# Performance work log

Hardware: AMD Instinct MI355X
Metric: run time of the kernel (lower is better)

## Reference

```python
import jax, jax.numpy as jnp
import numpy as np

N, E, D, H = 50000, 400000, 128, 256


def setup_inputs() -> dict:
    key = jax.random.key(0)
    ks = jax.random.split(key, 16)
    s = 0.02
    inp = {
        "x": jax.random.normal(ks[0], (N, D), dtype=jnp.float32),
        "edge_index": jax.random.randint(ks[1], (2, E), 0, N, dtype=jnp.int64),
        "steps": 1,
        # encoder MLP: Linear(D->H), Linear(H->H), relu after each
        "enc_w1": jax.random.normal(ks[2], (H, D), dtype=jnp.float32) * s,
        "enc_b1": jnp.zeros((H,), dtype=jnp.float32),
        "enc_w2": jax.random.normal(ks[3], (H, H), dtype=jnp.float32) * s,
        "enc_b2": jnp.zeros((H,), dtype=jnp.float32),
        # GeneralConv lin_msg (root_weight=False, bias=True)
        "msg_w": jax.random.normal(ks[4], (H, H), dtype=jnp.float32) * s,
        "msg_b": jnp.zeros((H,), dtype=jnp.float32),
        # decoder MLP: Linear(2H->H) relu, Linear(H->D) tanh
        "dec_w1": jax.random.normal(ks[5], (H, 2 * H), dtype=jnp.float32) * s,
        "dec_b1": jnp.zeros((H,), dtype=jnp.float32),
        "dec_w2": jax.random.normal(ks[6], (D, H), dtype=jnp.float32) * s,
        "dec_b2": jnp.zeros((D,), dtype=jnp.float32),
    }
    return inp


def reference(x, edge_index, steps, enc_w1, enc_b1, enc_w2, enc_b2,
              msg_w, msg_b, dec_w1, dec_b1, dec_w2, dec_b2):
    src = edge_index[0]
    dst = edge_index[1]
    n = x.shape[0]
    for _ in range(steps):  # steps is a small static python int
        # encoder MLP (batch_norm=False, dropout=0, relu + relu)
        h = jax.nn.relu(x @ enc_w1.T + enc_b1)
        h = jax.nn.relu(h @ enc_w2.T + enc_b2)
        # GeneralConv: message = lin_msg(x_j); aggr='add'; no root weight
        # lin_msg is edge-independent -> transform on nodes, then gather/scatter
        m = h @ msg_w.T + msg_b                      # [N, H]
        out = jax.ops.segment_sum(m[src], dst, num_segments=n)  # [N, H]
        # decoder on cat(out, h): relu then tanh
        d = jax.nn.relu(jnp.concatenate([out, h], axis=-1) @ dec_w1.T + dec_b1)
        x = jnp.tanh(d @ dec_w2.T + dec_b2)
    return x
```

## Files before the change

kernel.cpp:

```cpp
#include <hip/hip_runtime.h>
#include <cmath>


typedef __attribute__((ext_vector_type(8))) short  short8;
typedef __attribute__((ext_vector_type(4))) float  f32x4;
typedef __attribute__((ext_vector_type(4))) unsigned short us4;

typedef unsigned short u16;
typedef unsigned int   u32;

static __device__ __forceinline__ u16 f2bf(float f) {
    u32 u = __float_as_uint(f);
    u = (u + 0x7FFFu + ((u >> 16) & 1u)) >> 16;
    return (u16)u;
}
static __device__ __forceinline__ float bf2f(u16 h) {
    return __uint_as_float(((u32)h) << 16);
}

static __device__ __forceinline__ void g2l16(const void* g, void* l) {
    __builtin_amdgcn_global_load_lds(
        (const __attribute__((address_space(1))) u32*)g,
        (__attribute__((address_space(3))) u32*)l, 16, 0, 0);
}

__global__ __launch_bounds__(512, 2) void enc_fused(
    const u16* __restrict__ xb, const u16* __restrict__ w1,
    const float* __restrict__ b1, const u16* __restrict__ w2,
    const float* __restrict__ b2, const u16* __restrict__ wm,
    const float* __restrict__ bm, u16* __restrict__ hout,
    u16* __restrict__ mout, const int N)
{
    __shared__ u16 As[64 * 32];
    __shared__ u16 Ws[256 * 32];
    __shared__ u16 hL[8][64 * 32];

    const int t    = threadIdx.x;
    const int r0   = blockIdx.x * 64;
    const int wave = t >> 6;
    const int lane = t & 63;
    const int n    = lane & 15;
    const int q    = lane >> 4;
    const int wc   = wave * 32;
    const int lrow = lane >> 2;
    const int qofs = (lane & 3) * 8;

    const int arow = min(r0 + wave * 16 + lrow, N - 1);
    const u16* aptr = xb + (size_t)arow * 128 + qofs;
    const int wrA = wave * 16 + lrow;
    const int wrB = (wave + 8) * 16 + lrow;

    f32x4 acc[4][2];
#pragma unroll
    for (int i = 0; i < 4; i++)
#pragma unroll
        for (int j = 0; j < 2; j++) acc[i][j] = (f32x4)0.0f;

    for (int kc = 0; kc < 128; kc += 32) {
        __syncthreads();
        if (wave < 4) g2l16(aptr + kc, &As[wave * 512]);
        g2l16(w1 + (size_t)wrA * 128 + kc + qofs, &Ws[wave * 512]);
        g2l16(w1 + (size_t)wrB * 128 + kc + qofs, &Ws[(wave + 8) * 512]);
        __syncthreads();
        short8 af[4], bf[2];
#pragma unroll
        for (int i = 0; i < 4; i++)
            af[i] = *reinterpret_cast<const short8*>(&As[(i * 16 + n) * 32 + q * 8]);
#pragma unroll
        for (int j = 0; j < 2; j++)
            bf[j] = *reinterpret_cast<const short8*>(&Ws[(wc + j * 16 + n) * 32 + q * 8]);
#pragma unroll
        for (int i = 0; i < 4; i++)
#pragma unroll
            for (int j = 0; j < 2; j++)
                acc[i][j] = __builtin_amdgcn_mfma_f32_16x16x32_bf16(
                    af[i], bf[j], acc[i][j], 0, 0, 0);
    }
    {
        float bv[2];
#pragma unroll
        for (int j = 0; j < 2; j++) bv[j] = b1[wc + j * 16 + n];
#pragma unroll
        for (int i = 0; i < 4; i++)
#pragma unroll
            for (int reg = 0; reg < 4; reg++) {
                const int row = i * 16 + q * 4 + reg;
#pragma unroll
                for (int j = 0; j < 2; j++) {
                    const float v = fmaxf(acc[i][j][reg] + bv[j], 0.0f);
                    hL[wave][row * 32 + j * 16 + n] = f2bf(v);
                }
            }
    }

#pragma unroll
    for (int i = 0; i < 4; i++)
#pragma unroll
        for (int j = 0; j < 2; j++) acc[i][j] = (f32x4)0.0f;
    for (int c = 0; c < 8; c++) {
        __syncthreads();
        g2l16(w2 + (size_t)wrA * 256 + c * 32 + qofs, &Ws[wave * 512]);
        g2l16(w2 + (size_t)wrB * 256 + c * 32 + qofs, &Ws[(wave + 8) * 512]);
        __syncthreads();
        short8 af[4], bf[2];
#pragma unroll
        for (int i = 0; i < 4; i++)
            af[i] = *reinterpret_cast<const short8*>(&hL[c][(i * 16 + n) * 32 + q * 8]);
#pragma unroll
        for (int j = 0; j < 2; j++)
            bf[j] = *reinterpret_cast<const short8*>(&Ws[(wc + j * 16 + n) * 32 + q * 8]);
#pragma unroll
        for (int i = 0; i < 4; i++)
#pragma unroll
            for (int j = 0; j < 2; j++)
                acc[i][j] = __builtin_amdgcn_mfma_f32_16x16x32_bf16(
                    af[i], bf[j], acc[i][j], 0, 0, 0);
    }
    {
        float bv[2];
#pragma unroll
        for (int j = 0; j < 2; j++) bv[j] = b2[wc + j * 16 + n];
#pragma unroll
        for (int i = 0; i < 4; i++)
#pragma unroll
            for (int reg = 0; reg < 4; reg++) {
                const int row = r0 + i * 16 + q * 4 + reg;
                if (row < N) {
#pragma unroll
                    for (int j = 0; j < 2; j++) {
                        const float v = fmaxf(acc[i][j][reg] + bv[j], 0.0f);
                        hout[(size_t)row * 256 + wc + j * 16 + n] = f2bf(v);
                    }
                }
            }
        __syncthreads();
#pragma unroll
        for (int i = 0; i < 4; i++)
#pragma unroll
            for (int reg = 0; reg < 4; reg++) {
                const int row = i * 16 + q * 4 + reg;
#pragma unroll
                for (int j = 0; j < 2; j++) {
                    const float v = fmaxf(acc[i][j][reg] + bv[j], 0.0f);
                    hL[wave][row * 32 + j * 16 + n] = f2bf(v);
                }
            }
    }

#pragma unroll
    for (int i = 0; i < 4; i++)
#pragma unroll
        for (int j = 0; j < 2; j++) acc[i][j] = (f32x4)0.0f;
    for (int c = 0; c < 8; c++) {
        __syncthreads();
        g2l16(wm + (size_t)wrA * 256 + c * 32 + qofs, &Ws[wave * 512]);
        g2l16(wm + (size_t)wrB * 256 + c * 32 + qofs, &Ws[(wave + 8) * 512]);
        __syncthreads();
        short8 af[4], bf[2];
#pragma unroll
        for (int i = 0; i < 4; i++)
            af[i] = *reinterpret_cast<const short8*>(&hL[c][(i * 16 + n) * 32 + q * 8]);
#pragma unroll
        for (int j = 0; j < 2; j++)
            bf[j] = *reinterpret_cast<const short8*>(&Ws[(wc + j * 16 + n) * 32 + q * 8]);
#pragma unroll
        for (int i = 0; i < 4; i++)
#pragma unroll
            for (int j = 0; j < 2; j++)
                acc[i][j] = __builtin_amdgcn_mfma_f32_16x16x32_bf16(
                    af[i], bf[j], acc[i][j], 0, 0, 0);
    }
    {
        float bv[2];
#pragma unroll
        for (int j = 0; j < 2; j++) bv[j] = bm[wc + j * 16 + n];
#pragma unroll
        for (int i = 0; i < 4; i++)
#pragma unroll
            for (int reg = 0; reg < 4; reg++) {
                const int row = r0 + i * 16 + q * 4 + reg;
                if (row < N) {
#pragma unroll
                    for (int j = 0; j < 2; j++)
                        mout[(size_t)row * 256 + wc + j * 16 + n] =
                            f2bf(acc[i][j][reg] + bv[j]);
                }
            }
    }
}

__global__ __launch_bounds__(512, 2) void dec_fused(
    const u16* __restrict__ aggr, const u16* __restrict__ h,
    const u16* __restrict__ wd1, const float* __restrict__ bd1,
    const u16* __restrict__ wd2, const float* __restrict__ bd2,
    float* __restrict__ out, const int N)
{
    __shared__ u16 As[64 * 32];
    __shared__ u16 Ws[256 * 32];
    __shared__ u16 dL[8][64 * 32];

    const int t    = threadIdx.x;
    const int r0   = blockIdx.x * 64;
    const int wave = t >> 6;
    const int lane = t & 63;
    const int n    = lane & 15;
    const int q    = lane >> 4;
    const int wc   = wave * 32;
    const int lrow = lane >> 2;
    const int qofs = (lane & 3) * 8;

    const int arow = min(r0 + wave * 16 + lrow, N - 1);
    const u16* ap0 = aggr + (size_t)arow * 256 + qofs;
    const u16* ap1 = h    + (size_t)arow * 256 + qofs;
    const int wrA = wave * 16 + lrow;
    const int wrB = (wave + 8) * 16 + lrow;

    f32x4 acc[4][2];
#pragma unroll
    for (int i = 0; i < 4; i++)
#pragma unroll
        for (int j = 0; j < 2; j++) acc[i][j] = (f32x4)0.0f;

    for (int kc = 0; kc < 512; kc += 32) {
        __syncthreads();
        if (wave < 4) {
            if (kc < 256) g2l16(ap0 + kc, &As[wave * 512]);
            else          g2l16(ap1 + (kc - 256), &As[wave * 512]);
        }
        g2l16(wd1 + (size_t)wrA * 512 + kc + qofs, &Ws[wave * 512]);
        g2l16(wd1 + (size_t)wrB * 512 + kc + qofs, &Ws[(wave + 8) * 512]);
        __syncthreads();
        short8 af[4], bf[2];
#pragma unroll
        for (int i = 0; i < 4; i++)
            af[i] = *reinterpret_cast<const short8*>(&As[(i * 16 + n) * 32 + q * 8]);
#pragma unroll
        for (int j = 0; j < 2; j++)
            bf[j] = *reinterpret_cast<const short8*>(&Ws[(wc + j * 16 + n) * 32 + q * 8]);
#pragma unroll
        for (int i = 0; i < 4; i++)
#pragma unroll
            for (int j = 0; j < 2; j++)
                acc[i][j] = __builtin_amdgcn_mfma_f32_16x16x32_bf16(
                    af[i], bf[j], acc[i][j], 0, 0, 0);
    }
    {
        float bv[2];
#pragma unroll
        for (int j = 0; j < 2; j++) bv[j] = bd1[wc + j * 16 + n];
#pragma unroll
        for (int i = 0; i < 4; i++)
#pragma unroll
            for (int reg = 0; reg < 4; reg++) {
                const int row = i * 16 + q * 4 + reg;
#pragma unroll
                for (int j = 0; j < 2; j++) {
                    const float v = fmaxf(acc[i][j][reg] + bv[j], 0.0f);
                    dL[wave][row * 32 + j * 16 + n] = f2bf(v);
                }
            }
    }

    f32x4 acc2[4];
#pragma unroll
    for (int i = 0; i < 4; i++) acc2[i] = (f32x4)0.0f;
    const int wc2 = wave * 16;
    for (int c = 0; c < 8; c++) {
        __syncthreads();
        g2l16(wd2 + (size_t)(wave * 16 + lrow) * 256 + c * 32 + qofs,
              &Ws[wave * 512]);
        __syncthreads();
        short8 af[4], bf;
#pragma unroll
        for (int i = 0; i < 4; i++)
            af[i] = *reinterpret_cast<const short8*>(&dL[c][(i * 16 + n) * 32 + q * 8]);
        bf = *reinterpret_cast<const short8*>(&Ws[(wave * 16 + n) * 32 + q * 8]);
#pragma unroll
        for (int i = 0; i < 4; i++)
            acc2[i] = __builtin_amdgcn_mfma_f32_16x16x32_bf16(
                af[i], bf, acc2[i], 0, 0, 0);
    }
    {
        const float bv = bd2[wc2 + n];
#pragma unroll
        for (int i = 0; i < 4; i++)
#pragma unroll
            for (int reg = 0; reg < 4; reg++) {
                const int row = r0 + i * 16 + q * 4 + reg;
                if (row < N)
                    out[(size_t)row * 128 + wc2 + n] = tanhf(acc2[i][reg] + bv);
            }
    }
}

__global__ __launch_bounds__(256) void cvt7_kernel(
    const float* s0, const float* s1, const float* s2, const float* s3,
    const float* s4, const float* s5,
    u16* d0, u16* d1, u16* d2, u16* d3, u16* d4, u16* d5,
    int* __restrict__ zp,
    int n0, int n1, int n2, int n3, int n4, int n5, int nz)
{
    const int i = blockIdx.x * 256 + threadIdx.x;
    if (blockIdx.y == 6) {
        if (i < nz) zp[i] = 0;
        return;
    }
    const float* s; u16* d; int nq;
    switch (blockIdx.y) {
        case 0: s = s0; d = d0; nq = n0; break;
        case 1: s = s1; d = d1; nq = n1; break;
        case 2: s = s2; d = d2; nq = n2; break;
        case 3: s = s3; d = d3; nq = n3; break;
        case 4: s = s4; d = d4; nq = n4; break;
        default: s = s5; d = d5; nq = n5; break;
    }
    if (i < nq) {
        const float4 v = reinterpret_cast<const float4*>(s)[i];
        us4 o = { f2bf(v.x), f2bf(v.y), f2bf(v.z), f2bf(v.w) };
        reinterpret_cast<us4*>(d)[i] = o;
    }
}

__global__ __launch_bounds__(256) void fill_kernel(
    const int* __restrict__ ei, int* __restrict__ cursor,
    int* __restrict__ bucket, const int E, const int Nn)
{
    const int e = blockIdx.x * 256 + threadIdx.x;
    if (e < E) {
        const int src = ei[e];
        const int dst = ei[(size_t)E + e];
        if ((unsigned)dst < (unsigned)Nn) {
            const int pos = atomicAdd(&cursor[dst], 1);
            if (pos < 64) bucket[(size_t)dst * 64 + pos] = src;
        }
    }
}

__global__ __launch_bounds__(256) void gather_sum_kernel(
    const u16* __restrict__ m, const int* __restrict__ bucket,
    const int* __restrict__ cursor, u16* __restrict__ outa, const int Nn)
{
    const int wave = (int)((blockIdx.x * 256u + threadIdx.x) >> 6);
    const int lane = threadIdx.x & 63;
    if (wave >= Nn) return;
    const int cnt = min(cursor[wave], 64);
    const int* bl = bucket + (size_t)wave * 64;
    float a0 = 0.f, a1 = 0.f, a2 = 0.f, a3 = 0.f;
    int i = 0;
    for (; i + 3 < cnt; i += 4) {
        int sidx[4];
#pragma unroll
        for (int u = 0; u < 4; u++) sidx[u] = bl[i + u];
        us4 v[4];
#pragma unroll
        for (int u = 0; u < 4; u++) {
            const int s = ((unsigned)sidx[u] < (unsigned)Nn) ? sidx[u] : 0;
            v[u] = *reinterpret_cast<const us4*>(&m[(size_t)s * 256 + lane * 4]);
        }
#pragma unroll
        for (int u = 0; u < 4; u++) {
            if ((unsigned)sidx[u] < (unsigned)Nn) {
                a0 += bf2f(v[u].x); a1 += bf2f(v[u].y);
                a2 += bf2f(v[u].z); a3 += bf2f(v[u].w);
            }
        }
    }
    for (; i < cnt; i++) {
        const int s0 = bl[i];
        if ((unsigned)s0 < (unsigned)Nn) {
            const us4 v0 = *reinterpret_cast<const us4*>(
                &m[(size_t)s0 * 256 + lane * 4]);
            a0 += bf2f(v0.x); a1 += bf2f(v0.y);
            a2 += bf2f(v0.z); a3 += bf2f(v0.w);
        }
    }
    us4 o = { f2bf(a0), f2bf(a1), f2bf(a2), f2bf(a3) };
    *reinterpret_cast<us4*>(&outa[(size_t)wave * 256 + lane * 4]) = o;
}

extern "C" void kernel_launch(void* const* d_in, const int* in_sizes, int n_in,
                              void* d_out, int out_size, void* d_ws, size_t ws_size,
                              hipStream_t stream)
{
    const float* x      = (const float*)d_in[0];
    const int*   ei     = (const int*)d_in[1];
    const float* enc_w1 = (const float*)d_in[3];
    const float* enc_b1 = (const float*)d_in[4];
    const float* enc_w2 = (const float*)d_in[5];
    const float* enc_b2 = (const float*)d_in[6];
    const float* msg_w  = (const float*)d_in[7];
    const float* msg_b  = (const float*)d_in[8];
    const float* dec_w1 = (const float*)d_in[9];
    const float* dec_b1 = (const float*)d_in[10];
    const float* dec_w2 = (const float*)d_in[11];
    const float* dec_b2 = (const float*)d_in[12];

    const int N = 50000, D = 128, H = 256;
    const int E = in_sizes[1] / 2;

    u16* xb   = (u16*)d_ws;
    u16* h    = xb   + (size_t)N * D;
    u16* m    = h    + (size_t)N * H;
    u16* aggr = m    + (size_t)N * H;
    u16* w1   = aggr + (size_t)N * H;
    u16* w2   = w1 + 256 * 128;
    u16* wm   = w2 + 256 * 256;
    u16* wd1  = wm + 256 * 256;
    u16* wd2  = wd1 + 256 * 512;
    int* cursor = (int*)(wd2 + 128 * 256);
    int* bucket = cursor + N;

    const dim3 blk(256);
    const dim3 blk512(512);
    const int nb64 = (N + 63) / 64;

    cvt7_kernel<<<dim3((N * D / 4 + 255) / 256, 7), blk, 0, stream>>>(
        x, enc_w1, enc_w2, msg_w, dec_w1, dec_w2,
        xb, w1, w2, wm, wd1, wd2, cursor,
        N * D / 4, 256 * 128 / 4, 256 * 256 / 4, 256 * 256 / 4,
        256 * 512 / 4, 128 * 256 / 4, N);

    fill_kernel<<<dim3((E + 255) / 256), blk, 0, stream>>>(
        ei, cursor, bucket, E, N);

    enc_fused<<<dim3(nb64), blk512, 0, stream>>>(
        xb, w1, enc_b1, w2, enc_b2, wm, msg_b, h, m, N);

    gather_sum_kernel<<<dim3((N * 64 + 255) / 256), blk, 0, stream>>>(
        m, bucket, cursor, aggr, N);

    dec_fused<<<dim3(nb64), blk512, 0, stream>>>(
        aggr, h, wd1, dec_b1, wd2, dec_b2, (float*)d_out, N);
}
```

Measured before the change: 244.8 us.

## Fuse x fp32-to-bf16 conversion into encoder GEMM and widen gather batch

The encoder kernel now loads fp32 x tiles directly into LDS (reusing the hL buffer) and converts them to bf16 in registers before the MFMAs. This removes the separate conversion pass over x and the bf16 copy of x in the workspace. The conversion kernel now only handles the weights and the cursor zeroing, on a smaller grid. Separately, the gather-sum loop issues 8 predicated neighbor loads per iteration instead of 4 and drops the scalar tail loop. In exchange, the encoder's A-tile traffic doubles and it does extra conversion ALU work, and a barrier is added before hL is reused.

```diff
diff --git a/kernel.cpp b/kernel.cpp
--- a/kernel.cpp
+++ b/kernel.cpp
@@ -24,16 +24,23 @@
         (__attribute__((address_space(3))) u32*)l, 16, 0, 0);
 }
 
+static __device__ __forceinline__ short8 cvt8(const float* p) {
+    short8 r;
+#pragma unroll
+    for (int e = 0; e < 8; e++) r[e] = (short)f2bf(p[e]);
+    return r;
+}
+
 __global__ __launch_bounds__(512, 2) void enc_fused(
-    const u16* __restrict__ xb, const u16* __restrict__ w1,
+    const float* __restrict__ x, const u16* __restrict__ w1,
     const float* __restrict__ b1, const u16* __restrict__ w2,
     const float* __restrict__ b2, const u16* __restrict__ wm,
     const float* __restrict__ bm, u16* __restrict__ hout,
     u16* __restrict__ mout, const int N)
 {
-    __shared__ u16 As[64 * 32];
     __shared__ u16 Ws[256 * 32];
     __shared__ u16 hL[8][64 * 32];
+    float* AsF = (float*)&hL[0][0];
 
     const int t    = threadIdx.x;
     const int r0   = blockIdx.x * 64;
@@ -45,8 +52,9 @@
     const int lrow = lane >> 2;
     const int qofs = (lane & 3) * 8;
 
-    const int arow = min(r0 + wave * 16 + lrow, N - 1);
-    const u16* aptr = xb + (size_t)arow * 128 + qofs;
+    const int axrow = min(r0 + wave * 8 + (lane >> 3), N - 1);
+    const float* xp = x + (size_t)axrow * 128 + (lane & 7) * 4;
+
     const int wrA = wave * 16 + lrow;
     const int wrB = (wave + 8) * 16 + lrow;
 
@@ -56,16 +64,16 @@
 #pragma unroll
         for (int j = 0; j < 2; j++) acc[i][j] = (f32x4)0.0f;
 
-    for (int kc = 0; kc < 128; kc += 32) {
-        __syncthreads();
-        if (wave < 4) g2l16(aptr + kc, &As[wave * 512]);
-        g2l16(w1 + (size_t)wrA * 128 + kc + qofs, &Ws[wave * 512]);
-        g2l16(w1 + (size_t)wrB * 128 + kc + qofs, &Ws[(wave + 8) * 512]);
+    for (int c = 0; c < 4; c++) {
+        __syncthreads();
+        g2l16(xp + c * 32, &AsF[wave * 256]);
+        g2l16(w1 + (size_t)wrA * 128 + c * 32 + qofs, &Ws[wave * 512]);
+        g2l16(w1 + (size_t)wrB * 128 + c * 32 + qofs, &Ws[(wave + 8) * 512]);
         __syncthreads();
         short8 af[4], bf[2];
 #pragma unroll
         for (int i = 0; i < 4; i++)
-            af[i] = *reinterpret_cast<const short8*>(&As[(i * 16 + n) * 32 + q * 8]);
+            af[i] = cvt8(&AsF[(i * 16 + n) * 32 + q * 8]);
 #pragma unroll
         for (int j = 0; j < 2; j++)
             bf[j] = *reinterpret_cast<const short8*>(&Ws[(wc + j * 16 + n) * 32 + q * 8]);
@@ -76,6 +84,7 @@
                 acc[i][j] = __builtin_amdgcn_mfma_f32_16x16x32_bf16(
                     af[i], bf[j], acc[i][j], 0, 0, 0);
     }
+    __syncthreads();
     {
         float bv[2];
 #pragma unroll
@@ -293,15 +302,15 @@
     }
 }
 
-__global__ __launch_bounds__(256) void cvt7_kernel(
+__global__ __launch_bounds__(256) void cvt6_kernel(
     const float* s0, const float* s1, const float* s2, const float* s3,
-    const float* s4, const float* s5,
-    u16* d0, u16* d1, u16* d2, u16* d3, u16* d4, u16* d5,
+    const float* s4,
+    u16* d0, u16* d1, u16* d2, u16* d3, u16* d4,
     int* __restrict__ zp,
-    int n0, int n1, int n2, int n3, int n4, int n5, int nz)
+    int n0, int n1, int n2, int n3, int n4, int nz)
 {
     const int i = blockIdx.x * 256 + threadIdx.x;
-    if (blockIdx.y == 6) {
+    if (blockIdx.y == 5) {
         if (i < nz) zp[i] = 0;
         return;
     }
@@ -311,8 +320,7 @@
         case 1: s = s1; d = d1; nq = n1; break;
         case 2: s = s2; d = d2; nq = n2; break;
         case 3: s = s3; d = d3; nq = n3; break;
-        case 4: s = s4; d = d4; nq = n4; break;
-        default: s = s5; d = d5; nq = n5; break;
+        default: s = s4; d = d4; nq = n4; break;
     }
     if (i < nq) {
         const float4 v = reinterpret_cast<const float4*>(s)[i];
@@ -346,32 +354,23 @@
     const int cnt = min(cursor[wave], 64);
     const int* bl = bucket + (size_t)wave * 64;
     float a0 = 0.f, a1 = 0.f, a2 = 0.f, a3 = 0.f;
-    int i = 0;
-    for (; i + 3 < cnt; i += 4) {
-        int sidx[4];
-#pragma unroll
-        for (int u = 0; u < 4; u++) sidx[u] = bl[i + u];
-        us4 v[4];
-#pragma unroll
-        for (int u = 0; u < 4; u++) {
+    for (int base = 0; base < cnt; base += 8) {
+        int sidx[8];
+#pragma unroll
+        for (int u = 0; u < 8; u++)
+            sidx[u] = (base + u < cnt) ? bl[base + u] : -1;
+        us4 v[8];
+#pragma unroll
+        for (int u = 0; u < 8; u++) {
             const int s = ((unsigned)sidx[u] < (unsigned)Nn) ? sidx[u] : 0;
             v[u] = *reinterpret_cast<const us4*>(&m[(size_t)s * 256 + lane * 4]);
         }
 #pragma unroll
-        for (int u = 0; u < 4; u++) {
+        for (int u = 0; u < 8; u++) {
             if ((unsigned)sidx[u] < (unsigned)Nn) {
                 a0 += bf2f(v[u].x); a1 += bf2f(v[u].y);
                 a2 += bf2f(v[u].z); a3 += bf2f(v[u].w);
             }
-        }
-    }
-    for (; i < cnt; i++) {
-        const int s0 = bl[i];
-        if ((unsigned)s0 < (unsigned)Nn) {
-            const us4 v0 = *reinterpret_cast<const us4*>(
-                &m[(size_t)s0 * 256 + lane * 4]);
-            a0 += bf2f(v0.x); a1 += bf2f(v0.y);
-            a2 += bf2f(v0.z); a3 += bf2f(v0.w);
         }
     }
     us4 o = { f2bf(a0), f2bf(a1), f2bf(a2), f2bf(a3) };
@@ -398,8 +397,7 @@
     const int N = 50000, D = 128, H = 256;
     const int E = in_sizes[1] / 2;
 
-    u16* xb   = (u16*)d_ws;
-    u16* h    = xb   + (size_t)N * D;
+    u16* h    = (u16*)d_ws;
     u16* m    = h    + (size_t)N * H;
     u16* aggr = m    + (size_t)N * H;
     u16* w1   = aggr + (size_t)N * H;
@@ -413,18 +411,19 @@
     const dim3 blk(256);
     const dim3 blk512(512);
     const int nb64 = (N + 63) / 64;
-
-    cvt7_kernel<<<dim3((N * D / 4 + 255) / 256, 7), blk, 0, stream>>>(
-        x, enc_w1, enc_w2, msg_w, dec_w1, dec_w2,
-        xb, w1, w2, wm, wd1, wd2, cursor,
-        N * D / 4, 256 * 128 / 4, 256 * 256 / 4, 256 * 256 / 4,
+    const int cvtx = (N + 255) / 256;
+
+    cvt6_kernel<<<dim3(cvtx, 6), blk, 0, stream>>>(
+        enc_w1, enc_w2, msg_w, dec_w1, dec_w2,
+        w1, w2, wm, wd1, wd2, cursor,
+        256 * 128 / 4, 256 * 256 / 4, 256 * 256 / 4,
         256 * 512 / 4, 128 * 256 / 4, N);
 
     fill_kernel<<<dim3((E + 255) / 256), blk, 0, stream>>>(
         ei, cursor, bucket, E, N);
 
     enc_fused<<<dim3(nb64), blk512, 0, stream>>>(
-        xb, w1, enc_b1, w2, enc_b2, wm, msg_b, h, m, N);
+        x, w1, enc_b1, w2, enc_b2, wm, msg_b, h, m, N);
 
     gather_sum_kernel<<<dim3((N * 64 + 255) / 256), blk, 0, stream>>>(
         m, bucket, cursor, aggr, N);
```

New measurement: 238.6 us. 2.5% less time.
